# Performance work log

Hardware: AMD Instinct MI355X
Metric: run time of the kernel (lower is better)

## Reference

```python
import jax, jax.numpy as jnp
import numpy as np


def setup_inputs() -> dict:
    key = jax.random.key(0)
    k_x, k_g, k_fc, k_pj = jax.random.split(key, 4)
    B, T, C, H, E = 4, 2048, 1024, 2048, 8
    n_layer = 12
    x = jax.random.normal(k_x, (B, T, C), dtype=jnp.float32)
    w_gate = 0.02 * jax.random.normal(k_g, (C, E), dtype=jnp.float32)
    w_fc = 0.02 * jax.random.normal(k_fc, (C, H, E), dtype=jnp.float32)
    w_proj = (0.02 * (2 * n_layer) ** -0.5) * jax.random.normal(k_pj, (H, C, E), dtype=jnp.float32)
    return {"x": x, "w_gate": w_gate, "w_fc": w_fc, "w_proj": w_proj, "top_k": 2}


def reference(x, w_gate, w_fc, w_proj, top_k):
    # x: (B,T,C); w_gate: (C,E); w_fc: (C,H,E); w_proj: (H,C,E)
    E = w_gate.shape[-1]
    gate = jnp.einsum('btc,ce->bte', x, w_gate)                  # gating logits
    top_vals, top_idx = jax.lax.top_k(gate, top_k)               # (B,T,K) — raw logits used as combine weights (as in source)
    # Per-expert combine weight: sum_k top_val_k * onehot(idx_k) — zero for unselected experts.
    # This is mathematically identical to gathering the K expert weight slices per token
    # (the source's gather+einsum) but avoids the (B,T,C,H,K) weight blowup.
    onehot = jax.nn.one_hot(top_idx, E, dtype=x.dtype)           # (B,T,K,E)
    w_e = jnp.einsum('btk,btke->bte', top_vals, onehot)          # (B,T,E)
    h = jax.nn.silu(jnp.einsum('btc,che->bthe', x, w_fc))        # (B,T,H,E)
    o = jnp.einsum('bthe,bte,hce->btc', h, w_e, w_proj)          # weighted expert combine
    return o
```

## Files before the change

kernel.cpp:

```cpp
#include <hip/hip_runtime.h>
#include <hip/hip_bf16.h>


#define NTOK 8192
#define CD   1024
#define HD   2048
#define NE   8
#define NSLOT 16384
#define MTILES 32

typedef short  short8_t  __attribute__((ext_vector_type(8)));
typedef __bf16 bf16x8_t  __attribute__((ext_vector_type(8)));
typedef float  f32x4_t   __attribute__((ext_vector_type(4)));

struct FragArg {
  short8_t v;
  __device__ operator short8_t() const { return v; }
  __device__ operator bf16x8_t() const { return __builtin_bit_cast(bf16x8_t, v); }
};

static __device__ __forceinline__ float b2f(unsigned short u) {
  union { float f; unsigned int i; } w; w.i = ((unsigned int)u) << 16; return w.f;
}
static __device__ __forceinline__ unsigned short f2b(float f) {
  unsigned int u = __float_as_uint(f);
  u += 0x7fffu + ((u >> 16) & 1u);
  return (unsigned short)(u >> 16);
}
static __device__ __forceinline__ void gl2lds16(const void* g, void* l) {
  __builtin_amdgcn_global_load_lds((__attribute__((address_space(1))) void*)g,
                                   (__attribute__((address_space(3))) void*)l,
                                   16, 0, 0);
}
static __device__ __forceinline__ int swz(int row, int kc) {
  return row * 4 + (kc ^ ((row >> 1) & 3));
}

__global__ __launch_bounds__(256) void gate_kernel(
    const float* __restrict__ x, const float* __restrict__ wg,
    int* __restrict__ tok_e, float* __restrict__ tok_v)
{
  int wv = threadIdx.x >> 6, lane = threadIdx.x & 63;
  int tk = blockIdx.x * 4 + wv;
  const float* xr = x + (size_t)tk * CD;
  float acc[NE] = {0, 0, 0, 0, 0, 0, 0, 0};
  #pragma unroll
  for (int jj = 0; jj < 4; ++jj) {
    int c0 = (lane + 64 * jj) * 4;
    float4 xv = *(const float4*)(xr + c0);
    #pragma unroll
    for (int j = 0; j < 4; ++j) {
      float xf = (j == 0) ? xv.x : (j == 1) ? xv.y : (j == 2) ? xv.z : xv.w;
      const float* wr = wg + (size_t)(c0 + j) * NE;
      float4 w0 = *(const float4*)wr;
      float4 w1 = *(const float4*)(wr + 4);
      acc[0] += xf * w0.x; acc[1] += xf * w0.y;
      acc[2] += xf * w0.z; acc[3] += xf * w0.w;
      acc[4] += xf * w1.x; acc[5] += xf * w1.y;
      acc[6] += xf * w1.z; acc[7] += xf * w1.w;
    }
  }
  #pragma unroll
  for (int off = 32; off >= 1; off >>= 1)
    #pragma unroll
    for (int e = 0; e < NE; ++e) acc[e] += __shfl_down(acc[e], off, 64);
  if (lane == 0) {
    float v1 = -3.0e38f, v2 = -3.0e38f; int i1 = 0, i2 = 1;
    #pragma unroll
    for (int e = 0; e < NE; ++e) {
      float g = acc[e];
      if (g > v1) { v2 = v1; i2 = i1; v1 = g; i1 = e; }
      else if (g > v2) { v2 = g; i2 = e; }
    }
    tok_e[tk * 2] = i1; tok_e[tk * 2 + 1] = i2;
    tok_v[tk * 2] = v1; tok_v[tk * 2 + 1] = v2;
  }
}

__global__ __launch_bounds__(256) void router_kernel(
    const int* __restrict__ tok_e, const float* __restrict__ tok_v,
    int* __restrict__ g_counts, int* __restrict__ g_base,
    int* __restrict__ bucket_tok, float* __restrict__ bucket_v,
    int* __restrict__ slot_of)
{
  __shared__ int cnt[NE], bas[NE], cur[NE];
  int t = threadIdx.x;
  if (t < NE) { cnt[t] = 0; cur[t] = 0; }
  __syncthreads();
  for (int s = t; s < NSLOT; s += 256) atomicAdd(&cnt[tok_e[s]], 1);
  __syncthreads();
  if (t == 0) { int o = 0; for (int e = 0; e < NE; ++e) { bas[e] = o; o += cnt[e]; } }
  __syncthreads();
  if (t < NE) { g_counts[t] = cnt[t]; g_base[t] = bas[t]; }
  for (int s = t; s < NSLOT; s += 256) {
    int e = tok_e[s];
    int pos = atomicAdd(&cur[e], 1);
    int sl = bas[e] + pos;
    bucket_tok[sl] = s >> 1;
    bucket_v[sl]   = tok_v[s];
    slot_of[s]     = sl;
  }
}

__global__ __launch_bounds__(256) void cvt_x_kernel(
    const float* __restrict__ x, unsigned short* __restrict__ xb)
{
  int gid = blockIdx.x * 256 + threadIdx.x;
  const float* p = x + (size_t)gid * 8;
  float4 a = *(const float4*)p;
  float4 b = *(const float4*)(p + 4);
  short8_t o;
  o[0] = (short)f2b(a.x); o[1] = (short)f2b(a.y);
  o[2] = (short)f2b(a.z); o[3] = (short)f2b(a.w);
  o[4] = (short)f2b(b.x); o[5] = (short)f2b(b.y);
  o[6] = (short)f2b(b.z); o[7] = (short)f2b(b.w);
  *(short8_t*)(xb + (size_t)gid * 8) = o;
}

__global__ __launch_bounds__(256) void pack_kernel(
    const float* __restrict__ in, unsigned short* __restrict__ out,
    int D0, int D1)
{
  __shared__ __align__(16) unsigned short lds[NE * 32 * 40];
  int b1 = blockIdx.x * 32, b0 = blockIdx.y * 32;
  int t = threadIdx.x;
  int d1i = t & 31, d0q = t >> 5;
  #pragma unroll
  for (int r = 0; r < 4; ++r) {
    int d0i = d0q * 4 + r;
    const float* src = in + ((size_t)(b0 + d0i) * D1 + (b1 + d1i)) * NE;
    float4 v0 = *(const float4*)src;
    float4 v1 = *(const float4*)(src + 4);
    unsigned short* dst0 = &lds[0 * 32 * 40 + d1i * 40 + d0i];
    dst0[0 * 32 * 40] = f2b(v0.x);
    dst0[1 * 32 * 40] = f2b(v0.y);
    dst0[2 * 32 * 40] = f2b(v0.z);
    dst0[3 * 32 * 40] = f2b(v0.w);
    dst0[4 * 32 * 40] = f2b(v1.x);
    dst0[5 * 32 * 40] = f2b(v1.y);
    dst0[6 * 32 * 40] = f2b(v1.z);
    dst0[7 * 32 * 40] = f2b(v1.w);
  }
  __syncthreads();
  int dchunk = t & 3, d1w = (t >> 2) & 31, ehalf = t >> 7;
  #pragma unroll
  for (int p = 0; p < 4; ++p) {
    int e = ehalf + 2 * p;
    short8_t v = *(const short8_t*)&lds[e * 32 * 40 + d1w * 40 + dchunk * 8];
    *(short8_t*)(out + ((size_t)e * D1 + (b1 + d1w)) * D0 + b0 + dchunk * 8) = v;
  }
}

__global__ __launch_bounds__(256) void gemm1_kernel(
    const unsigned short* __restrict__ xb, const unsigned short* __restrict__ wfcp,
    const int* __restrict__ g_counts, const int* __restrict__ g_base,
    const int* __restrict__ bucket_tok, const float* __restrict__ bucket_v,
    unsigned short* __restrict__ hbuf)
{
  int e = blockIdx.z, mt = blockIdx.y, nt = blockIdx.x;
  int cnt = g_counts[e];
  int m0 = mt * 128;
  if (m0 >= cnt) return;
  int base = g_base[e];
  int n0 = nt * 128;

  __shared__ __align__(16) unsigned short lsA[128 * 32];
  __shared__ __align__(16) unsigned short lsB[128 * 32];
  __shared__ int   s_tok[128];
  __shared__ float s_v[128];

  int t = threadIdx.x;
  if (t < 128) {
    int ok = (m0 + t) < cnt;
    s_tok[t] = ok ? bucket_tok[base + m0 + t] : 0;
    s_v[t]   = ok ? bucket_v[base + m0 + t] : 0.0f;
  }
  __syncthreads();

  int slot = t & 3;
  int r0 = t >> 2, r1 = r0 + 64;
  int gc0 = slot ^ ((r0 >> 1) & 3);
  int gc1 = slot ^ ((r1 >> 1) & 3);
  const unsigned short* gA0 = xb + (size_t)s_tok[r0] * CD + gc0 * 8;
  const unsigned short* gA1 = xb + (size_t)s_tok[r1] * CD + gc1 * 8;
  const unsigned short* gB0 = wfcp + ((size_t)e * HD + n0 + r0) * CD + gc0 * 8;
  const unsigned short* gB1 = wfcp + ((size_t)e * HD + n0 + r1) * CD + gc1 * 8;
  unsigned short* lA0 = &lsA[(size_t)t * 8];
  unsigned short* lA1 = &lsA[(size_t)(256 + t) * 8];
  unsigned short* lB0 = &lsB[(size_t)t * 8];
  unsigned short* lB1 = &lsB[(size_t)(256 + t) * 8];

  int lane = t & 63, wv = t >> 6;
  int wm = (wv & 1) * 64, wn = (wv >> 1) * 64;
  int ml = lane & 15, kq = lane >> 4;

  f32x4_t acc[4][4];
  #pragma unroll
  for (int i = 0; i < 4; ++i)
    #pragma unroll
    for (int j = 0; j < 4; ++j) acc[i][j] = (f32x4_t){0.f, 0.f, 0.f, 0.f};

  for (int k0 = 0; k0 < CD; k0 += 32) {
    __syncthreads();
    gl2lds16(gA0 + k0, lA0);
    gl2lds16(gA1 + k0, lA1);
    gl2lds16(gB0 + k0, lB0);
    gl2lds16(gB1 + k0, lB1);
    __syncthreads();
    short8_t af[4], bfr[4];
    #pragma unroll
    for (int i = 0; i < 4; ++i) {
      int ar = wm + i * 16 + ml;
      af[i]  = *(const short8_t*)&lsA[swz(ar, kq) * 8];
      int br = wn + i * 16 + ml;
      bfr[i] = *(const short8_t*)&lsB[swz(br, kq) * 8];
    }
    #pragma unroll
    for (int i = 0; i < 4; ++i)
      #pragma unroll
      for (int j = 0; j < 4; ++j)
        acc[i][j] = __builtin_amdgcn_mfma_f32_16x16x32_bf16(
            FragArg{af[i]}, FragArg{bfr[j]}, acc[i][j], 0, 0, 0);
  }

  #pragma unroll
  for (int i = 0; i < 4; ++i) {
    int rb = wm + i * 16 + kq * 4;
    #pragma unroll
    for (int r = 0; r < 4; ++r) {
      int row = rb + r;
      if (m0 + row < cnt) {
        float v = s_v[row];
        size_t ro = (size_t)(base + m0 + row) * HD + n0;
        #pragma unroll
        for (int j = 0; j < 4; ++j) {
          float z = acc[i][j][r];
          float val = v * (z / (1.0f + __expf(-z)));
          hbuf[ro + wn + j * 16 + ml] = f2b(val);
        }
      }
    }
  }
}

__global__ __launch_bounds__(256) void gemm2_kernel(
    const unsigned short* __restrict__ hbuf, const unsigned short* __restrict__ wpjp,
    const int* __restrict__ g_counts, const int* __restrict__ g_base,
    unsigned short* __restrict__ oslot)
{
  int e = blockIdx.z, mt = blockIdx.y, nt = blockIdx.x;
  int cnt = g_counts[e];
  int m0 = mt * 128;
  if (m0 >= cnt) return;
  int base = g_base[e];
  int n0 = nt * 128;

  __shared__ __align__(16) unsigned short lsA[128 * 32];
  __shared__ __align__(16) unsigned short lsB[128 * 32];

  int t = threadIdx.x;
  int slot = t & 3;
  int r0 = t >> 2, r1 = r0 + 64;
  int gc0 = slot ^ ((r0 >> 1) & 3);
  int gc1 = slot ^ ((r1 >> 1) & 3);
  const unsigned short* gA0 = hbuf + (size_t)(base + m0 + r0) * HD + gc0 * 8;
  const unsigned short* gA1 = hbuf + (size_t)(base + m0 + r1) * HD + gc1 * 8;
  const unsigned short* gB0 = wpjp + ((size_t)e * CD + n0 + r0) * HD + gc0 * 8;
  const unsigned short* gB1 = wpjp + ((size_t)e * CD + n0 + r1) * HD + gc1 * 8;
  unsigned short* lA0 = &lsA[(size_t)t * 8];
  unsigned short* lA1 = &lsA[(size_t)(256 + t) * 8];
  unsigned short* lB0 = &lsB[(size_t)t * 8];
  unsigned short* lB1 = &lsB[(size_t)(256 + t) * 8];

  int lane = t & 63, wv = t >> 6;
  int wm = (wv & 1) * 64, wn = (wv >> 1) * 64;
  int ml = lane & 15, kq = lane >> 4;

  f32x4_t acc[4][4];
  #pragma unroll
  for (int i = 0; i < 4; ++i)
    #pragma unroll
    for (int j = 0; j < 4; ++j) acc[i][j] = (f32x4_t){0.f, 0.f, 0.f, 0.f};

  for (int k0 = 0; k0 < HD; k0 += 32) {
    __syncthreads();
    gl2lds16(gA0 + k0, lA0);
    gl2lds16(gA1 + k0, lA1);
    gl2lds16(gB0 + k0, lB0);
    gl2lds16(gB1 + k0, lB1);
    __syncthreads();
    short8_t af[4], bfr[4];
    #pragma unroll
    for (int i = 0; i < 4; ++i) {
      int ar = wm + i * 16 + ml;
      af[i]  = *(const short8_t*)&lsA[swz(ar, kq) * 8];
      int br = wn + i * 16 + ml;
      bfr[i] = *(const short8_t*)&lsB[swz(br, kq) * 8];
    }
    #pragma unroll
    for (int i = 0; i < 4; ++i)
      #pragma unroll
      for (int j = 0; j < 4; ++j)
        acc[i][j] = __builtin_amdgcn_mfma_f32_16x16x32_bf16(
            FragArg{af[i]}, FragArg{bfr[j]}, acc[i][j], 0, 0, 0);
  }

  #pragma unroll
  for (int i = 0; i < 4; ++i) {
    int rb = wm + i * 16 + kq * 4;
    #pragma unroll
    for (int r = 0; r < 4; ++r) {
      int row = rb + r;
      if (m0 + row < cnt) {
        size_t ro = (size_t)(base + m0 + row) * CD + n0;
        #pragma unroll
        for (int j = 0; j < 4; ++j)
          oslot[ro + wn + j * 16 + ml] = f2b(acc[i][j][r]);
      }
    }
  }
}

__global__ __launch_bounds__(256) void combine_kernel(
    const unsigned short* __restrict__ oslot, const int* __restrict__ slot_of,
    float* __restrict__ out)
{
  int gid = blockIdx.x * 256 + threadIdx.x;
  int tk = gid >> 7;
  int ch = (gid & 127) * 8;
  int s0 = slot_of[tk * 2], s1 = slot_of[tk * 2 + 1];
  short8_t a = *(const short8_t*)(oslot + (size_t)s0 * CD + ch);
  short8_t b = *(const short8_t*)(oslot + (size_t)s1 * CD + ch);
  float* op = out + (size_t)tk * CD + ch;
  float4 o0, o1;
  o0.x = b2f((unsigned short)a[0]) + b2f((unsigned short)b[0]);
  o0.y = b2f((unsigned short)a[1]) + b2f((unsigned short)b[1]);
  o0.z = b2f((unsigned short)a[2]) + b2f((unsigned short)b[2]);
  o0.w = b2f((unsigned short)a[3]) + b2f((unsigned short)b[3]);
  o1.x = b2f((unsigned short)a[4]) + b2f((unsigned short)b[4]);
  o1.y = b2f((unsigned short)a[5]) + b2f((unsigned short)b[5]);
  o1.z = b2f((unsigned short)a[6]) + b2f((unsigned short)b[6]);
  o1.w = b2f((unsigned short)a[7]) + b2f((unsigned short)b[7]);
  *(float4*)op = o0;
  *(float4*)(op + 4) = o1;
}

extern "C" void kernel_launch(void* const* d_in, const int* in_sizes, int n_in,
                              void* d_out, int out_size, void* d_ws, size_t ws_size,
                              hipStream_t stream)
{
  const float* x   = (const float*)d_in[0];
  const float* wg  = (const float*)d_in[1];
  const float* wfc = (const float*)d_in[2];
  const float* wpj = (const float*)d_in[3];
  float* out = (float*)d_out;

  char* w = (char*)d_ws;
  unsigned short* wfcp  = (unsigned short*)w; w += (size_t)NE * HD * CD * 2;
  unsigned short* wpjp  = (unsigned short*)w; w += (size_t)NE * CD * HD * 2;
  unsigned short* xb    = (unsigned short*)w; w += (size_t)NTOK * CD * 2;
  unsigned short* hbuf  = (unsigned short*)w; w += (size_t)NSLOT * HD * 2;
  unsigned short* oslot = (unsigned short*)w; w += (size_t)NSLOT * CD * 2;
  int*   tok_e      = (int*)w;   w += NSLOT * 4;
  float* tok_v      = (float*)w; w += NSLOT * 4;
  int*   slot_of    = (int*)w;   w += NSLOT * 4;
  int*   bucket_tok = (int*)w;   w += NSLOT * 4;
  float* bucket_v   = (float*)w; w += NSLOT * 4;
  int*   g_counts   = (int*)w;   w += 256;
  int*   g_base     = (int*)w;   w += 256;

  pack_kernel<<<dim3(HD / 32, CD / 32), 256, 0, stream>>>(wfc, wfcp, CD, HD);
  pack_kernel<<<dim3(CD / 32, HD / 32), 256, 0, stream>>>(wpj, wpjp, HD, CD);
  cvt_x_kernel<<<(NTOK * CD / 8) / 256, 256, 0, stream>>>(x, xb);
  gate_kernel<<<NTOK / 4, 256, 0, stream>>>(x, wg, tok_e, tok_v);
  router_kernel<<<1, 256, 0, stream>>>(tok_e, tok_v, g_counts, g_base,
                                       bucket_tok, bucket_v, slot_of);
  gemm1_kernel<<<dim3(HD / 128, MTILES, NE), 256, 0, stream>>>(
      xb, wfcp, g_counts, g_base, bucket_tok, bucket_v, hbuf);
  gemm2_kernel<<<dim3(CD / 128, MTILES, NE), 256, 0, stream>>>(
      hbuf, wpjp, g_counts, g_base, oslot);
  combine_kernel<<<(NTOK * CD / 8) / 256, 256, 0, stream>>>(oslot, slot_of, out);
}
```

Baseline: 498.1 us.

## Fuse x conversion into gating, parallelize router scan, merge packs, XCD-aware GEMM order

Folds the fp32-to-bf16 conversion of x into the gate kernel so x is read only once, and merges the two weight-pack launches into a single launch split on blockIdx.z. The single-block router now gives each thread a contiguous chunk of slots and computes per-expert prefix sums with wavefront shuffles instead of contending on shared-memory atomics, which also makes slot order deterministic. Both expert GEMMs switch to a 1D grid with an index remap that sends consecutive M-tiles of the same expert to different XCDs, aiming at better L2 reuse of weight tiles. The remap relies on exact divisibility of the tile counts and adds index arithmetic per block.

```diff
diff --git a/kernel.cpp b/kernel.cpp
--- a/kernel.cpp
+++ b/kernel.cpp
@@ -9,6 +9,7 @@
 #define NSLOT 16384
 #define MTILES 32
 
+typedef short  short4_t  __attribute__((ext_vector_type(4)));
 typedef short  short8_t  __attribute__((ext_vector_type(8)));
 typedef __bf16 bf16x8_t  __attribute__((ext_vector_type(8)));
 typedef float  f32x4_t   __attribute__((ext_vector_type(4)));
@@ -38,16 +39,22 @@
 
 __global__ __launch_bounds__(256) void gate_kernel(
     const float* __restrict__ x, const float* __restrict__ wg,
+    unsigned short* __restrict__ xb,
     int* __restrict__ tok_e, float* __restrict__ tok_v)
 {
   int wv = threadIdx.x >> 6, lane = threadIdx.x & 63;
   int tk = blockIdx.x * 4 + wv;
   const float* xr = x + (size_t)tk * CD;
+  unsigned short* xbr = xb + (size_t)tk * CD;
   float acc[NE] = {0, 0, 0, 0, 0, 0, 0, 0};
   #pragma unroll
   for (int jj = 0; jj < 4; ++jj) {
     int c0 = (lane + 64 * jj) * 4;
     float4 xv = *(const float4*)(xr + c0);
+    short4_t ob;
+    ob[0] = (short)f2b(xv.x); ob[1] = (short)f2b(xv.y);
+    ob[2] = (short)f2b(xv.z); ob[3] = (short)f2b(xv.w);
+    *(short4_t*)(xbr + c0) = ob;
     #pragma unroll
     for (int j = 0; j < 4; ++j) {
       float xf = (j == 0) ? xv.x : (j == 1) ? xv.y : (j == 2) ? xv.z : xv.w;
@@ -83,46 +90,56 @@
     int* __restrict__ bucket_tok, float* __restrict__ bucket_v,
     int* __restrict__ slot_of)
 {
-  __shared__ int cnt[NE], bas[NE], cur[NE];
+  __shared__ int cnts[NE][256];
+  __shared__ int bas[NE], tot[NE];
   int t = threadIdx.x;
-  if (t < NE) { cnt[t] = 0; cur[t] = 0; }
+  int local[NE] = {0, 0, 0, 0, 0, 0, 0, 0};
+  for (int i = 0; i < 64; ++i) local[tok_e[t * 64 + i]]++;
+  #pragma unroll
+  for (int e = 0; e < NE; ++e) cnts[e][t] = local[e];
   __syncthreads();
-  for (int s = t; s < NSLOT; s += 256) atomicAdd(&cnt[tok_e[s]], 1);
+  int lane = t & 63, wv = t >> 6;
+  for (int e = wv; e < NE; e += 4) {
+    int carry = 0;
+    #pragma unroll
+    for (int c = 0; c < 4; ++c) {
+      int v = cnts[e][c * 64 + lane];
+      int incl = v;
+      #pragma unroll
+      for (int off = 1; off < 64; off <<= 1) {
+        int n = __shfl_up(incl, off, 64);
+        if (lane >= off) incl += n;
+      }
+      cnts[e][c * 64 + lane] = incl - v + carry;
+      carry += __shfl(incl, 63, 64);
+    }
+    if (lane == 0) tot[e] = carry;
+  }
   __syncthreads();
-  if (t == 0) { int o = 0; for (int e = 0; e < NE; ++e) { bas[e] = o; o += cnt[e]; } }
+  if (t == 0) { int o = 0; for (int e = 0; e < NE; ++e) { bas[e] = o; o += tot[e]; } }
   __syncthreads();
-  if (t < NE) { g_counts[t] = cnt[t]; g_base[t] = bas[t]; }
-  for (int s = t; s < NSLOT; s += 256) {
+  if (t < NE) { g_counts[t] = tot[t]; g_base[t] = bas[t]; }
+  for (int i = 0; i < 64; ++i) {
+    int s = t * 64 + i;
     int e = tok_e[s];
-    int pos = atomicAdd(&cur[e], 1);
-    int sl = bas[e] + pos;
+    int sl = bas[e] + cnts[e][t];
+    cnts[e][t]++;
     bucket_tok[sl] = s >> 1;
     bucket_v[sl]   = tok_v[s];
     slot_of[s]     = sl;
   }
 }
 
-__global__ __launch_bounds__(256) void cvt_x_kernel(
-    const float* __restrict__ x, unsigned short* __restrict__ xb)
-{
-  int gid = blockIdx.x * 256 + threadIdx.x;
-  const float* p = x + (size_t)gid * 8;
-  float4 a = *(const float4*)p;
-  float4 b = *(const float4*)(p + 4);
-  short8_t o;
-  o[0] = (short)f2b(a.x); o[1] = (short)f2b(a.y);
-  o[2] = (short)f2b(a.z); o[3] = (short)f2b(a.w);
-  o[4] = (short)f2b(b.x); o[5] = (short)f2b(b.y);
-  o[6] = (short)f2b(b.z); o[7] = (short)f2b(b.w);
-  *(short8_t*)(xb + (size_t)gid * 8) = o;
-}
-
 __global__ __launch_bounds__(256) void pack_kernel(
-    const float* __restrict__ in, unsigned short* __restrict__ out,
-    int D0, int D1)
+    const float* __restrict__ wfc, const float* __restrict__ wpj,
+    unsigned short* __restrict__ wfcp, unsigned short* __restrict__ wpjp)
 {
   __shared__ __align__(16) unsigned short lds[NE * 32 * 40];
-  int b1 = blockIdx.x * 32, b0 = blockIdx.y * 32;
+  const float* in; unsigned short* out; int D0, D1, b0, b1;
+  if (blockIdx.z == 0) { in = wfc; out = wfcp; D0 = CD; D1 = HD;
+                         b1 = blockIdx.x * 32; b0 = blockIdx.y * 32; }
+  else                 { in = wpj; out = wpjp; D0 = HD; D1 = CD;
+                         b1 = blockIdx.y * 32; b0 = blockIdx.x * 32; }
   int t = threadIdx.x;
   int d1i = t & 31, d0q = t >> 5;
   #pragma unroll
@@ -131,7 +148,7 @@
     const float* src = in + ((size_t)(b0 + d0i) * D1 + (b1 + d1i)) * NE;
     float4 v0 = *(const float4*)src;
     float4 v1 = *(const float4*)(src + 4);
-    unsigned short* dst0 = &lds[0 * 32 * 40 + d1i * 40 + d0i];
+    unsigned short* dst0 = &lds[d1i * 40 + d0i];
     dst0[0 * 32 * 40] = f2b(v0.x);
     dst0[1 * 32 * 40] = f2b(v0.y);
     dst0[2 * 32 * 40] = f2b(v0.z);
@@ -157,7 +174,13 @@
     const int* __restrict__ bucket_tok, const float* __restrict__ bucket_v,
     unsigned short* __restrict__ hbuf)
 {
-  int e = blockIdx.z, mt = blockIdx.y, nt = blockIdx.x;
+  int id = blockIdx.x;
+  int xcd = id & 7;
+  int r = id >> 3;
+  int nt = r & 15;
+  int emt = (r >> 4) * 8 + xcd;
+  int e = emt >> 5, mt = emt & 31;
+
   int cnt = g_counts[e];
   int m0 = mt * 128;
   if (m0 >= cnt) return;
@@ -210,10 +233,8 @@
     short8_t af[4], bfr[4];
     #pragma unroll
     for (int i = 0; i < 4; ++i) {
-      int ar = wm + i * 16 + ml;
-      af[i]  = *(const short8_t*)&lsA[swz(ar, kq) * 8];
-      int br = wn + i * 16 + ml;
-      bfr[i] = *(const short8_t*)&lsB[swz(br, kq) * 8];
+      af[i]  = *(const short8_t*)&lsA[swz(wm + i * 16 + ml, kq) * 8];
+      bfr[i] = *(const short8_t*)&lsB[swz(wn + i * 16 + ml, kq) * 8];
     }
     #pragma unroll
     for (int i = 0; i < 4; ++i)
@@ -227,14 +248,14 @@
   for (int i = 0; i < 4; ++i) {
     int rb = wm + i * 16 + kq * 4;
     #pragma unroll
-    for (int r = 0; r < 4; ++r) {
-      int row = rb + r;
+    for (int r2 = 0; r2 < 4; ++r2) {
+      int row = rb + r2;
       if (m0 + row < cnt) {
         float v = s_v[row];
         size_t ro = (size_t)(base + m0 + row) * HD + n0;
         #pragma unroll
         for (int j = 0; j < 4; ++j) {
-          float z = acc[i][j][r];
+          float z = acc[i][j][r2];
           float val = v * (z / (1.0f + __expf(-z)));
           hbuf[ro + wn + j * 16 + ml] = f2b(val);
         }
@@ -248,7 +269,13 @@
     const int* __restrict__ g_counts, const int* __restrict__ g_base,
     unsigned short* __restrict__ oslot)
 {
-  int e = blockIdx.z, mt = blockIdx.y, nt = blockIdx.x;
+  int id = blockIdx.x;
+  int xcd = id & 7;
+  int r = id >> 3;
+  int nt = r & 7;
+  int emt = (r >> 3) * 8 + xcd;
+  int e = emt >> 5, mt = emt & 31;
+
   int cnt = g_counts[e];
   int m0 = mt * 128;
   if (m0 >= cnt) return;
@@ -292,10 +319,8 @@
     short8_t af[4], bfr[4];
     #pragma unroll
     for (int i = 0; i < 4; ++i) {
-      int ar = wm + i * 16 + ml;
-      af[i]  = *(const short8_t*)&lsA[swz(ar, kq) * 8];
-      int br = wn + i * 16 + ml;
-      bfr[i] = *(const short8_t*)&lsB[swz(br, kq) * 8];
+      af[i]  = *(const short8_t*)&lsA[swz(wm + i * 16 + ml, kq) * 8];
+      bfr[i] = *(const short8_t*)&lsB[swz(wn + i * 16 + ml, kq) * 8];
     }
     #pragma unroll
     for (int i = 0; i < 4; ++i)
@@ -309,13 +334,13 @@
   for (int i = 0; i < 4; ++i) {
     int rb = wm + i * 16 + kq * 4;
     #pragma unroll
-    for (int r = 0; r < 4; ++r) {
-      int row = rb + r;
+    for (int r2 = 0; r2 < 4; ++r2) {
+      int row = rb + r2;
       if (m0 + row < cnt) {
         size_t ro = (size_t)(base + m0 + row) * CD + n0;
         #pragma unroll
         for (int j = 0; j < 4; ++j)
-          oslot[ro + wn + j * 16 + ml] = f2b(acc[i][j][r]);
+          oslot[ro + wn + j * 16 + ml] = f2b(acc[i][j][r2]);
       }
     }
   }
@@ -369,15 +394,13 @@
   int*   g_counts   = (int*)w;   w += 256;
   int*   g_base     = (int*)w;   w += 256;
 
-  pack_kernel<<<dim3(HD / 32, CD / 32), 256, 0, stream>>>(wfc, wfcp, CD, HD);
-  pack_kernel<<<dim3(CD / 32, HD / 32), 256, 0, stream>>>(wpj, wpjp, HD, CD);
-  cvt_x_kernel<<<(NTOK * CD / 8) / 256, 256, 0, stream>>>(x, xb);
-  gate_kernel<<<NTOK / 4, 256, 0, stream>>>(x, wg, tok_e, tok_v);
+  gate_kernel<<<NTOK / 4, 256, 0, stream>>>(x, wg, xb, tok_e, tok_v);
   router_kernel<<<1, 256, 0, stream>>>(tok_e, tok_v, g_counts, g_base,
                                        bucket_tok, bucket_v, slot_of);
-  gemm1_kernel<<<dim3(HD / 128, MTILES, NE), 256, 0, stream>>>(
+  pack_kernel<<<dim3(HD / 32, CD / 32, 2), 256, 0, stream>>>(wfc, wpj, wfcp, wpjp);
+  gemm1_kernel<<<(HD / 128) * MTILES * NE, 256, 0, stream>>>(
       xb, wfcp, g_counts, g_base, bucket_tok, bucket_v, hbuf);
-  gemm2_kernel<<<dim3(CD / 128, MTILES, NE), 256, 0, stream>>>(
+  gemm2_kernel<<<(CD / 128) * MTILES * NE, 256, 0, stream>>>(
       hbuf, wpjp, g_counts, g_base, oslot);
   combine_kernel<<<(NTOK * CD / 8) / 256, 256, 0, stream>>>(oslot, slot_of, out);
 }
```

Result: faster. 478.4 us (-4.0%).
